# Performance work log

Hardware: AMD Instinct MI355X
Metric: run time of the kernel (lower is better)

The kernel has to match this reference:

```python
import jax, jax.numpy as jnp
import numpy as np
import math

HEAD_DIM = 128
NUM_HEADS = 16
ROPE_BASE = 10000.0


def _rope(x, st_pos):
    # x: [B, S, H, hd], interleaved even/odd rotation as in the torch module
    S, hd = x.shape[1], x.shape[3]
    theta = 1.0 / (ROPE_BASE ** (jnp.arange(0, hd, 2, dtype=jnp.float32) / hd))  # [hd/2]
    pos = jnp.arange(st_pos, st_pos + S, dtype=jnp.float32)[:, None]             # [S,1]
    ang = pos * theta                                                            # [S, hd/2]
    sin = jnp.sin(ang)[None, :, None, :]
    cos = jnp.cos(ang)[None, :, None, :]
    xe, xo = x[..., 0::2], x[..., 1::2]
    re = xe * cos - xo * sin
    ro = xe * sin + xo * cos
    # re-interleave: stack pairs then flatten last two dims
    return jnp.stack([re, ro], axis=-1).reshape(x.shape)


def setup_inputs() -> dict:
    key = jax.random.key(0)
    ks = jax.random.split(key, 6)
    B, S, D = 4, 2048, 2048
    scale = 1.0 / math.sqrt(D)
    x = jax.random.normal(ks[0], (B, S, D), dtype=jnp.float32)
    # causal additive mask (prefill)
    mask = jnp.where(jnp.tril(jnp.ones((S, S), dtype=bool)), 0.0, -1e9).astype(jnp.float32)
    Wq = jax.random.normal(ks[1], (D, NUM_HEADS * HEAD_DIM), dtype=jnp.float32) * scale
    Wk = jax.random.normal(ks[2], (D, NUM_HEADS * HEAD_DIM), dtype=jnp.float32) * scale
    Wv = jax.random.normal(ks[3], (D, NUM_HEADS * HEAD_DIM), dtype=jnp.float32) * scale
    Wo = jax.random.normal(ks[4], (NUM_HEADS * HEAD_DIM, D), dtype=jnp.float32) * scale
    return {"x": x, "mask": mask, "Wq": Wq, "Wk": Wk, "Wv": Wv, "Wo": Wo, "st_pos": 0}


def reference(x, mask, Wq, Wk, Wv, Wo, st_pos):
    B, S, D = x.shape
    H, hd = NUM_HEADS, HEAD_DIM
    q = (x @ Wq).reshape(B, S, H, hd)
    k = (x @ Wk).reshape(B, S, H, hd)
    v = (x @ Wv).reshape(B, S, H, hd)
    q = _rope(q, st_pos)
    k = _rope(k, st_pos)
    # st_pos=0 prefill: cache slice == current k, v; n_rep == 1 (n_kv_heads=num_heads)
    scores = jnp.einsum('bqhd,bkhd->bhqk', q, k) / math.sqrt(hd)
    if mask is not None:
        scores = scores + mask
    attn = jax.nn.softmax(scores, axis=-1)
    a = jnp.einsum('bhqk,bkhd->bqhd', attn, v).reshape(B, S, H * hd)
    return a @ Wo
```

## Files before the change

kernel.cpp:

```cpp
#include <hip/hip_runtime.h>
#include <hip/hip_fp16.h>

typedef _Float16 f16;
typedef __attribute__((ext_vector_type(2))) _Float16 f16x2;
typedef __attribute__((ext_vector_type(4))) _Float16 f16x4v;
typedef __attribute__((ext_vector_type(8))) _Float16 f16x8;
typedef __attribute__((ext_vector_type(4))) float f32x4;

#define DEV __device__ __forceinline__

static constexpr int S_ = 2048;
static constexpr int D_ = 2048;
static constexpr int H_ = 16;
static constexpr int HD_ = 128;
static constexpr int B_ = 4;

typedef const __attribute__((address_space(1))) void* gptr_t;
typedef __attribute__((address_space(3))) void* lptr_t;

DEV void gl_lds16(const void* gsrc, void* lds) {
  __builtin_amdgcn_global_load_lds((gptr_t)gsrc, (lptr_t)lds, 16, 0, 0);
}

__global__ __launch_bounds__(256) void cvt_f32_to_f16(const float* __restrict__ in,
                                                      f16* __restrict__ out, long n) {
  long i0 = ((long)blockIdx.x * 256 + threadIdx.x) * 4;
  long stride = (long)gridDim.x * 256 * 4;
  for (long i = i0; i < n; i += stride) {
    float4 v = *(const float4*)(in + i);
    f16x4v o;
    o[0] = (f16)v.x; o[1] = (f16)v.y; o[2] = (f16)v.z; o[3] = (f16)v.w;
    *(f16x4v*)(out + i) = o;
  }
}

__global__ __launch_bounds__(256) void wtrans4(const float* __restrict__ W0, const float* __restrict__ W1,
                                               const float* __restrict__ W2, const float* __restrict__ W3,
                                               f16* __restrict__ Wt) {
  __shared__ float tile[32][33];
  int wi = blockIdx.y;
  const float* W = wi == 0 ? W0 : wi == 1 ? W1 : wi == 2 ? W2 : W3;
  f16* dst = Wt + (size_t)wi * D_ * D_;
  int bx = blockIdx.x & 63, by = blockIdx.x >> 6;
  int r0 = by << 5, c0 = bx << 5;
  int tx = threadIdx.x & 31, ty = threadIdx.x >> 5;
#pragma unroll
  for (int i = 0; i < 4; i++) {
    int r = ty + i * 8;
    tile[r][tx] = W[(size_t)(r0 + r) * D_ + c0 + tx];
  }
  __syncthreads();
#pragma unroll
  for (int i = 0; i < 4; i++) {
    int r = ty + i * 8;
    dst[(size_t)(c0 + r) * D_ + r0 + tx] = (f16)tile[tx][r];
  }
}

DEV f16x8 lds_frag(const f16* half, int row, int s, int lg) {
  int byte = row * 128 + s * 64 + lg * 16;
  byte ^= (row & 4) << 3;
  return *(const f16x8*)((const char*)half + byte);
}

template <typename CT>
__global__ __launch_bounds__(512, 2) void gemm8(const f16* __restrict__ A, const f16* __restrict__ Bt,
                                                CT* __restrict__ C, int M, int N, int K) {
  __shared__ alignas(16) f16 As[2][2][128 * 64];
  __shared__ alignas(16) f16 Bs[2][2][128 * 64];
  int nbx = N >> 8;
  int nwg = (M >> 8) * nbx;
  int bid = blockIdx.x;
  int wg = (bid & 7) * (nwg >> 3) + (bid >> 3);
  int bx = wg % nbx, by = wg / nbx;
  int tid = threadIdx.x, w = tid >> 6, l = tid & 63;
  int wm = w >> 2, wn = w & 3, lg = l >> 4, ln = l & 15;
  int nt = K >> 6;
  const f16* Ab = A + (size_t)(by * 256) * K;
  const f16* Bb = Bt + (size_t)(bx * 256) * K;

  auto stage = [&](const f16* src0, int kt, f16* dst) {
#pragma unroll
    for (int j = 0; j < 2; j++) {
      int c = j * 8 + w;
      int row = c * 8 + (l >> 3);
      int scol = ((l & 7) * 8) ^ ((row & 4) << 2);
      gl_lds16(src0 + (size_t)row * K + kt * 64 + scol, (char*)dst + c * 1024);
    }
  };

  f32x4 acc[8][4] = {};

  stage(Ab, 0, As[0][0]);
  stage(Ab + (size_t)128 * K, 0, As[0][1]);
  stage(Bb, 0, Bs[0][0]);
  stage(Bb + (size_t)128 * K, 0, Bs[0][1]);
  if (nt > 1) {
    stage(Bb, 1, Bs[1][0]);
    stage(Bb + (size_t)128 * K, 1, Bs[1][1]);
  }

  for (int t = 0; t < nt; t++) {
    if (t + 2 < nt) asm volatile("s_waitcnt vmcnt(4)" ::: "memory");
    else            asm volatile("s_waitcnt vmcnt(0)" ::: "memory");
    __builtin_amdgcn_s_barrier();
    asm volatile("" ::: "memory");
    const f16* Ah = As[t & 1][wm];
    const f16* Bh = Bs[t & 1][wn >> 1];
    int br0 = (wn & 1) * 64;
    f16x8 a[4], b0[4], b1[4];
#pragma unroll
    for (int i = 0; i < 4; i++) a[i] = lds_frag(Ah, i * 16 + ln, 0, lg);
#pragma unroll
    for (int i = 0; i < 4; i++) b0[i] = lds_frag(Bh, br0 + i * 16 + ln, 0, lg);
    if (t + 1 < nt) stage(Ab, t + 1, As[(t + 1) & 1][0]);
    __builtin_amdgcn_s_barrier();
    asm volatile("" ::: "memory");
    __builtin_amdgcn_s_setprio(1);
#pragma unroll
    for (int mi = 0; mi < 4; mi++)
#pragma unroll
      for (int ni = 0; ni < 4; ni++)
        acc[mi][ni] = __builtin_amdgcn_mfma_f32_16x16x32_f16(a[mi], b0[ni], acc[mi][ni], 0, 0, 0);
    __builtin_amdgcn_s_setprio(0);
    __builtin_amdgcn_s_barrier();
    asm volatile("" ::: "memory");
#pragma unroll
    for (int i = 0; i < 4; i++) a[i] = lds_frag(Ah, i * 16 + ln, 1, lg);
#pragma unroll
    for (int i = 0; i < 4; i++) b1[i] = lds_frag(Bh, br0 + i * 16 + ln, 1, lg);
    if (t + 1 < nt) stage(Ab + (size_t)128 * K, t + 1, As[(t + 1) & 1][1]);
    __builtin_amdgcn_s_barrier();
    asm volatile("" ::: "memory");
    __builtin_amdgcn_s_setprio(1);
#pragma unroll
    for (int mi = 0; mi < 4; mi++)
#pragma unroll
      for (int ni = 0; ni < 4; ni++)
        acc[mi][ni] = __builtin_amdgcn_mfma_f32_16x16x32_f16(a[mi], b1[ni], acc[mi][ni], 0, 0, 0);
    __builtin_amdgcn_s_setprio(0);
    __builtin_amdgcn_s_barrier();
    asm volatile("" ::: "memory");
#pragma unroll
    for (int i = 0; i < 4; i++) a[i] = lds_frag(Ah, 64 + i * 16 + ln, 0, lg);
    if (t + 2 < nt) stage(Bb, t + 2, Bs[t & 1][0]);
    __builtin_amdgcn_s_barrier();
    asm volatile("" ::: "memory");
    __builtin_amdgcn_s_setprio(1);
#pragma unroll
    for (int mi = 0; mi < 4; mi++)
#pragma unroll
      for (int ni = 0; ni < 4; ni++)
        acc[mi + 4][ni] = __builtin_amdgcn_mfma_f32_16x16x32_f16(a[mi], b0[ni], acc[mi + 4][ni], 0, 0, 0);
    __builtin_amdgcn_s_setprio(0);
    __builtin_amdgcn_s_barrier();
    asm volatile("" ::: "memory");
#pragma unroll
    for (int i = 0; i < 4; i++) a[i] = lds_frag(Ah, 64 + i * 16 + ln, 1, lg);
    if (t + 2 < nt) stage(Bb + (size_t)128 * K, t + 2, Bs[t & 1][1]);
    __builtin_amdgcn_s_barrier();
    asm volatile("" ::: "memory");
    __builtin_amdgcn_s_setprio(1);
#pragma unroll
    for (int mi = 0; mi < 4; mi++)
#pragma unroll
      for (int ni = 0; ni < 4; ni++)
        acc[mi + 4][ni] = __builtin_amdgcn_mfma_f32_16x16x32_f16(a[mi], b1[ni], acc[mi + 4][ni], 0, 0, 0);
    __builtin_amdgcn_s_setprio(0);
    __builtin_amdgcn_s_barrier();
    asm volatile("" ::: "memory");
  }

  int row0 = by * 256 + wm * 128;
  int col0 = bx * 256 + wn * 64;
#pragma unroll
  for (int mi = 0; mi < 8; mi++)
#pragma unroll
    for (int ni = 0; ni < 4; ni++)
#pragma unroll
      for (int r4 = 0; r4 < 4; r4++) {
        int row = row0 + mi * 16 + lg * 4 + r4;
        int col = col0 + ni * 16 + ln;
        float o = acc[mi][ni][r4];
        if constexpr (sizeof(CT) == 2) {
          float oo = __shfl_xor(o, 1);
          if (!(ln & 1)) {
            f16x2 pp; pp[0] = (f16)o; pp[1] = (f16)oo;
            *(f16x2*)(&C[(size_t)row * N + col]) = pp;
          }
        } else {
          C[(size_t)row * N + col] = o;
        }
      }
}

__global__ __launch_bounds__(256) void rope_table(float2* __restrict__ tab, const int* __restrict__ st) {
  int i = blockIdx.x * 256 + threadIdx.x;
  int s = i >> 6, j = i & 63;
  float theta = powf(10000.f, -(float)j / 64.f);
  float ang = (float)(s + st[0]) * theta;
  tab[i] = make_float2(cosf(ang), sinf(ang));
}

__global__ __launch_bounds__(256) void rope_apply(f16* __restrict__ X, const float2* __restrict__ tab,
                                                  float scale, long npairs) {
  long i0 = (long)blockIdx.x * 256 + threadIdx.x;
  long stride = (long)gridDim.x * 256;
  for (long p = i0; p < npairs; p += stride) {
    long row = p >> 10;
    int jp = (int)(p & 1023);
    int s = (int)(row & (S_ - 1));
    float2 cs = tab[s * 64 + (jp & 63)];
    f16x2 v = *(const f16x2*)(X + 2 * p);
    float xe = (float)v[0], xo = (float)v[1];
    float re = (xe * cs.x - xo * cs.y) * scale;
    float ro = (xe * cs.y + xo * cs.x) * scale;
    f16x2 o; o[0] = (f16)re; o[1] = (f16)ro;
    *(f16x2*)(X + 2 * p) = o;
  }
}

__global__ __launch_bounds__(256) void vtrans2(const f16* __restrict__ V, f16* __restrict__ VT2) {
  __shared__ alignas(16) f16 tile[64 * 128];
  int t = blockIdx.x, bh = blockIdx.y, b = bh >> 4, h = bh & 15;
  int tid = threadIdx.x, w = tid >> 6, l = tid & 63, lg = l >> 4, ln = l & 15;
  const f16* src = V + ((size_t)(b * S_ + t * 64) * H_ + h) * HD_;
#pragma unroll
  for (int i = 0; i < 4; i++) {
    int idx = i * 256 + tid;
    int r = idx >> 4, c8 = idx & 15;
    int c8s = c8 ^ ((r >> 3) & 3);
    *(f16x8*)(&tile[r * 128 + c8s * 8]) = *(const f16x8*)(src + (size_t)r * (H_ * HD_) + c8 * 8);
  }
  __syncthreads();
  f16* dst = VT2 + (size_t)(bh * 32 + t) * 16 * 512;
#pragma unroll
  for (int ci = 0; ci < 4; ci++) {
    int c = w * 4 + ci;
    int nj = c >> 1, kk = c & 1;
    f16x8 v;
#pragma unroll
    for (int e = 0; e < 8; e++) {
      int r = kk * 32 + lg * 8 + e;
      int col = nj * 16 + ln;
      int c8s = (col >> 3) ^ ((r >> 3) & 3);
      v[e] = tile[r * 128 + c8s * 8 + (col & 7)];
    }
    *(f16x8*)(dst + (size_t)c * 512 + l * 8) = v;
  }
}

__global__ __launch_bounds__(512, 4) void attn(const f16* __restrict__ Q, const f16* __restrict__ K,
                                               const f16* __restrict__ VT2, f16* __restrict__ O,
                                               const float2* __restrict__ tab) {
  __shared__ alignas(16) f16 kls[2][64 * 128];
  int id = blockIdx.x;
  int r8 = id & 7, j = id >> 3;
  int u = j & 7, g = j >> 3;
  int bh = r8 + (g << 3);
  int b = bh >> 4, h = bh & 15;
  int tid = threadIdx.x, w = tid >> 6, l = tid & 63, lg = l >> 4, ln = l & 15;

  const float QSCALE = 0.12751744910173355f;
  const f16* kp = K + (size_t)(b * S_) * D_ + h * HD_;
  const f16* vp2 = VT2 + (size_t)bh * 32 * 16 * 512;

  auto stageK = [&](int buf, int kv0) {
#pragma unroll
    for (int jj = 0; jj < 2; jj++) {
      int i = jj * 8 + w;
      int byte = i * 1024 + 16 * l;
      int r = byte >> 8;
      int c = ((byte >> 4) & 15) ^ (r & 7);
      gl_lds16(kp + (size_t)(kv0 + r) * D_ + c * 8, (char*)kls[buf] + i * 1024);
    }
  };

  int slo = ln + (((lg * 2) & 3) << 4);
  int shi = ln + (((lg * 2 + 1) & 3) << 4);
  int sel = (lg >> 1) & 1;

#pragma unroll 1
  for (int pi = 0; pi < 2; pi++) {
    int qsel = pi ? u : 15 - u;
    int q0 = qsel << 7;
    int qrow = q0 + w * 16 + ln;
    const f16* qp = Q + (size_t)(b * S_ + qrow) * D_ + h * HD_;
    const float2* tq = tab + (size_t)qrow * 64;
    f16x8 qf[4];
#pragma unroll
    for (int kc = 0; kc < 4; kc++) {
      f16x8 q = *(const f16x8*)(qp + kc * 32 + lg * 8);
#pragma unroll
      for (int p = 0; p < 4; p++) {
        float2 cs = tq[kc * 16 + lg * 4 + p];
        float e0 = (float)q[2 * p], e1 = (float)q[2 * p + 1];
        q[2 * p] = (f16)((e0 * cs.x - e1 * cs.y) * QSCALE);
        q[2 * p + 1] = (f16)((e0 * cs.y + e1 * cs.x) * QSCALE);
      }
      qf[kc] = q;
    }

    float m = -1e30f, lsum = 0.f;
    f32x4 oacc[8] = {};

    int nt = (q0 >> 6) + 2;
    if (pi) __syncthreads();
    stageK(0, 0);
    for (int t = 0; t < nt; t++) {
      int kv0 = t << 6;
      int cur = t & 1;
      __syncthreads();
      if (t + 1 < nt) stageK(cur ^ 1, (t + 1) << 6);
      if (kv0 > q0 + w * 16 + 15) continue;
      const f16* kb = kls[cur];
      const f16* vt = vp2 + (size_t)t * 16 * 512;

      f16x8 vfa[8];
#pragma unroll
      for (int c = 0; c < 8; c++) vfa[c] = *(const f16x8*)(vt + c * 512 + l * 8);

      f32x4 sf[4];
      __builtin_amdgcn_s_setprio(1);
#pragma unroll
      for (int ni = 0; ni < 4; ni++) {
        int n = ni * 16 + ln;
        f32x4 s = {0.f, 0.f, 0.f, 0.f};
#pragma unroll
        for (int kc = 0; kc < 4; kc++) {
          int mch = kc * 4 + lg;
          f16x8 kf = *(const f16x8*)(&kb[n * 128 + ((mch ^ (n & 7)) << 3)]);
          s = __builtin_amdgcn_mfma_f32_16x16x32_f16(kf, qf[kc], s, 0, 0, 0);
        }
        sf[ni] = s;
      }
      __builtin_amdgcn_s_setprio(0);

      if (t >= nt - 2) {
#pragma unroll
        for (int ni = 0; ni < 4; ni++) {
          int kvg = kv0 + ni * 16 + lg * 4;
#pragma unroll
          for (int r4 = 0; r4 < 4; r4++)
            if (kvg + r4 > qrow) sf[ni][r4] = -1e30f;
        }
      }
      float pm = fmaxf(fmaxf(fmaxf(sf[0][0], sf[0][1]), fmaxf(sf[0][2], sf[0][3])),
                       fmaxf(fmaxf(sf[1][0], sf[1][1]), fmaxf(sf[1][2], sf[1][3])));
      pm = fmaxf(pm, fmaxf(fmaxf(fmaxf(sf[2][0], sf[2][1]), fmaxf(sf[2][2], sf[2][3])),
                           fmaxf(fmaxf(sf[3][0], sf[3][1]), fmaxf(sf[3][2], sf[3][3]))));
      pm = fmaxf(pm, __shfl_xor(pm, 16));
      pm = fmaxf(pm, __shfl_xor(pm, 32));
      float scl = 1.f;
      bool defer = __all(pm <= m + 8.f);
      if (!defer) {
        float mn = fmaxf(m, pm);
        scl = __builtin_amdgcn_exp2f(m - mn);
        m = mn;
      }
      float rsum = 0.f;
#pragma unroll
      for (int ni = 0; ni < 4; ni++)
#pragma unroll
        for (int r4 = 0; r4 < 4; r4++) {
          float p = __builtin_amdgcn_exp2f(sf[ni][r4] - m);
          sf[ni][r4] = p;
          rsum += p;
        }
      lsum = lsum * scl + rsum;

      f16x4v hp[4];
#pragma unroll
      for (int ni = 0; ni < 4; ni++) {
        hp[ni][0] = (f16)sf[ni][0]; hp[ni][1] = (f16)sf[ni][1];
        hp[ni][2] = (f16)sf[ni][2]; hp[ni][3] = (f16)sf[ni][3];
      }
      if (!defer) {
#pragma unroll
        for (int nj = 0; nj < 8; nj++)
#pragma unroll
          for (int r4 = 0; r4 < 4; r4++) oacc[nj][r4] *= scl;
      }

      f16x8 pa[2];
#pragma unroll
      for (int kk = 0; kk < 2; kk++) {
        int2 e = __builtin_bit_cast(int2, hp[2 * kk]);
        int2 o = __builtin_bit_cast(int2, hp[2 * kk + 1]);
        int t0x = __shfl(e.x, slo), t0y = __shfl(e.y, slo);
        int t1x = __shfl(o.x, slo), t1y = __shfl(o.y, slo);
        int t2x = __shfl(e.x, shi), t2y = __shfl(e.y, shi);
        int t3x = __shfl(o.x, shi), t3y = __shfl(o.y, shi);
        int2 lo, hi;
        lo.x = sel ? t1x : t0x; lo.y = sel ? t1y : t0y;
        hi.x = sel ? t3x : t2x; hi.y = sel ? t3y : t2y;
        f16x4v plo = __builtin_bit_cast(f16x4v, lo);
        f16x4v phi = __builtin_bit_cast(f16x4v, hi);
        f16x8 p;
        p[0] = plo[0]; p[1] = plo[1]; p[2] = plo[2]; p[3] = plo[3];
        p[4] = phi[0]; p[5] = phi[1]; p[6] = phi[2]; p[7] = phi[3];
        pa[kk] = p;
      }

      __builtin_amdgcn_s_setprio(1);
#pragma unroll
      for (int kk = 0; kk < 2; kk++)
#pragma unroll
        for (int nj = 0; nj < 4; nj++)
          oacc[nj] = __builtin_amdgcn_mfma_f32_16x16x32_f16(vfa[nj * 2 + kk], pa[kk], oacc[nj], 0, 0, 0);
#pragma unroll
      for (int njb = 0; njb < 2; njb++) {
        f16x8 vf[4];
#pragma unroll
        for (int jj = 0; jj < 2; jj++)
#pragma unroll
          for (int kk = 0; kk < 2; kk++)
            vf[jj * 2 + kk] = *(const f16x8*)(vt + (size_t)(((4 + njb * 2 + jj) * 2 + kk) * 512) + l * 8);
#pragma unroll
        for (int kk = 0; kk < 2; kk++)
#pragma unroll
          for (int jj = 0; jj < 2; jj++)
            oacc[4 + njb * 2 + jj] = __builtin_amdgcn_mfma_f32_16x16x32_f16(
                vf[jj * 2 + kk], pa[kk], oacc[4 + njb * 2 + jj], 0, 0, 0);
      }
      __builtin_amdgcn_s_setprio(0);
    }

    lsum += __shfl_xor(lsum, 16);
    lsum += __shfl_xor(lsum, 32);
    f16* op = O + (size_t)(b * S_ + qrow) * D_ + h * HD_;
    float inv = 1.f / lsum;
#pragma unroll
    for (int nj = 0; nj < 8; nj++) {
      f16x4v ov;
#pragma unroll
      for (int r4 = 0; r4 < 4; r4++) ov[r4] = (f16)(oacc[nj][r4] * inv);
      *(f16x4v*)(op + nj * 16 + lg * 4) = ov;
    }
  }
}

extern "C" void kernel_launch(void* const* d_in, const int* in_sizes, int n_in,
                              void* d_out, int out_size, void* d_ws, size_t ws_size,
                              hipStream_t stream) {
  (void)in_sizes; (void)n_in; (void)out_size; (void)ws_size;
  const float* x = (const float*)d_in[0];
  const float* Wq = (const float*)d_in[2];
  const float* Wk = (const float*)d_in[3];
  const float* Wv = (const float*)d_in[4];
  const float* Wo = (const float*)d_in[5];
  const int* stp = (const int*)d_in[6];
  float* out = (float*)d_out;

  const size_t MS = (size_t)B_ * S_;
  f16* xh = (f16*)d_ws;
  f16* wqt = xh + MS * D_;
  f16* wkt = wqt + (size_t)D_ * D_;
  f16* wvt = wkt + (size_t)D_ * D_;
  f16* wot = wvt + (size_t)D_ * D_;
  f16* qh = wot + (size_t)D_ * D_;
  f16* kh = qh + MS * D_;
  f16* vh = kh + MS * D_;
  float2* tab = (float2*)(vh + MS * D_);
  f16* vt2 = xh;
  f16* aoh = vh;

  cvt_f32_to_f16<<<16384, 256, 0, stream>>>(x, xh, (long)(MS * D_));
  wtrans4<<<dim3(4096, 4), 256, 0, stream>>>(Wq, Wk, Wv, Wo, wqt);
  gemm8<f16><<<256, 512, 0, stream>>>(xh, wqt, qh, 8192, 2048, 2048);
  gemm8<f16><<<256, 512, 0, stream>>>(xh, wkt, kh, 8192, 2048, 2048);
  gemm8<f16><<<256, 512, 0, stream>>>(xh, wvt, vh, 8192, 2048, 2048);
  rope_table<<<512, 256, 0, stream>>>(tab, stp);
  rope_apply<<<4096, 256, 0, stream>>>(kh, tab, 1.0f, (long)(MS * 1024));
  vtrans2<<<dim3(32, 64), 256, 0, stream>>>(vh, vt2);
  attn<<<512, 512, 0, stream>>>(qh, kh, vt2, aoh, tab);
  gemm8<float><<<256, 512, 0, stream>>>(aoh, wot, out, 8192, 2048, 2048);
}
```

Measured before the change: 474.3 us.

## Fuse K RoPE into GEMM epilogue and load K directly from global in attention

```diff
diff --git a/kernel.cpp b/kernel.cpp
--- a/kernel.cpp
+++ b/kernel.cpp
@@ -20,6 +20,10 @@
 
 DEV void gl_lds16(const void* gsrc, void* lds) {
   __builtin_amdgcn_global_load_lds((gptr_t)gsrc, (lptr_t)lds, 16, 0, 0);
+}
+
+DEV int cvt_pk_i32(float a, float b) {
+  return __builtin_bit_cast(int, __builtin_amdgcn_cvt_pkrtz(a, b));
 }
 
 __global__ __launch_bounds__(256) void cvt_f32_to_f16(const float* __restrict__ in,
@@ -63,9 +67,10 @@
   return *(const f16x8*)((const char*)half + byte);
 }
 
-template <typename CT>
+template <typename CT, bool ROPE>
 __global__ __launch_bounds__(512, 2) void gemm8(const f16* __restrict__ A, const f16* __restrict__ Bt,
-                                                CT* __restrict__ C, int M, int N, int K) {
+                                                CT* __restrict__ C, int M, int N, int K,
+                                                const float2* __restrict__ tab) {
   __shared__ alignas(16) f16 As[2][2][128 * 64];
   __shared__ alignas(16) f16 Bs[2][2][128 * 64];
   int nbx = N >> 8;
@@ -185,7 +190,16 @@
         if constexpr (sizeof(CT) == 2) {
           float oo = __shfl_xor(o, 1);
           if (!(ln & 1)) {
-            f16x2 pp; pp[0] = (f16)o; pp[1] = (f16)oo;
+            f16x2 pp;
+            if constexpr (ROPE) {
+              int s = row & (S_ - 1);
+              int jp = (col & 127) >> 1;
+              float2 cs = tab[s * 64 + jp];
+              pp[0] = (f16)(o * cs.x - oo * cs.y);
+              pp[1] = (f16)(o * cs.y + oo * cs.x);
+            } else {
+              pp[0] = (f16)o; pp[1] = (f16)oo;
+            }
             *(f16x2*)(&C[(size_t)row * N + col]) = pp;
           }
         } else {
@@ -200,24 +214,6 @@
   float theta = powf(10000.f, -(float)j / 64.f);
   float ang = (float)(s + st[0]) * theta;
   tab[i] = make_float2(cosf(ang), sinf(ang));
-}
-
-__global__ __launch_bounds__(256) void rope_apply(f16* __restrict__ X, const float2* __restrict__ tab,
-                                                  float scale, long npairs) {
-  long i0 = (long)blockIdx.x * 256 + threadIdx.x;
-  long stride = (long)gridDim.x * 256;
-  for (long p = i0; p < npairs; p += stride) {
-    long row = p >> 10;
-    int jp = (int)(p & 1023);
-    int s = (int)(row & (S_ - 1));
-    float2 cs = tab[s * 64 + (jp & 63)];
-    f16x2 v = *(const f16x2*)(X + 2 * p);
-    float xe = (float)v[0], xo = (float)v[1];
-    float re = (xe * cs.x - xo * cs.y) * scale;
-    float ro = (xe * cs.y + xo * cs.x) * scale;
-    f16x2 o; o[0] = (f16)re; o[1] = (f16)ro;
-    *(f16x2*)(X + 2 * p) = o;
-  }
 }
 
 __global__ __launch_bounds__(256) void vtrans2(const f16* __restrict__ V, f16* __restrict__ VT2) {
@@ -253,7 +249,6 @@
 __global__ __launch_bounds__(512, 4) void attn(const f16* __restrict__ Q, const f16* __restrict__ K,
                                                const f16* __restrict__ VT2, f16* __restrict__ O,
                                                const float2* __restrict__ tab) {
-  __shared__ alignas(16) f16 kls[2][64 * 128];
   int id = blockIdx.x;
   int r8 = id & 7, j = id >> 3;
   int u = j & 7, g = j >> 3;
@@ -264,17 +259,6 @@
   const float QSCALE = 0.12751744910173355f;
   const f16* kp = K + (size_t)(b * S_) * D_ + h * HD_;
   const f16* vp2 = VT2 + (size_t)bh * 32 * 16 * 512;
-
-  auto stageK = [&](int buf, int kv0) {
-#pragma unroll
-    for (int jj = 0; jj < 2; jj++) {
-      int i = jj * 8 + w;
-      int byte = i * 1024 + 16 * l;
-      int r = byte >> 8;
-      int c = ((byte >> 4) & 15) ^ (r & 7);
-      gl_lds16(kp + (size_t)(kv0 + r) * D_ + c * 8, (char*)kls[buf] + i * 1024);
-    }
-  };
 
   int slo = ln + (((lg * 2) & 3) << 4);
   int shi = ln + (((lg * 2 + 1) & 3) << 4);
@@ -304,39 +288,35 @@
     float m = -1e30f, lsum = 0.f;
     f32x4 oacc[8] = {};
 
-    int nt = (q0 >> 6) + 2;
-    if (pi) __syncthreads();
-    stageK(0, 0);
-    for (int t = 0; t < nt; t++) {
+    int wnt = ((q0 + w * 16 + 15) >> 6) + 1;
+    for (int t = 0; t < wnt; t++) {
       int kv0 = t << 6;
-      int cur = t & 1;
-      __syncthreads();
-      if (t + 1 < nt) stageK(cur ^ 1, (t + 1) << 6);
-      if (kv0 > q0 + w * 16 + 15) continue;
-      const f16* kb = kls[cur];
       const f16* vt = vp2 + (size_t)t * 16 * 512;
 
       f16x8 vfa[8];
 #pragma unroll
-      for (int c = 0; c < 8; c++) vfa[c] = *(const f16x8*)(vt + c * 512 + l * 8);
+      for (int c = 0; c < 4; c++) vfa[c] = *(const f16x8*)(vt + c * 512 + l * 8);
 
       f32x4 sf[4];
+#pragma unroll
+      for (int ni = 0; ni < 4; ni++) sf[ni] = f32x4{0.f, 0.f, 0.f, 0.f};
       __builtin_amdgcn_s_setprio(1);
 #pragma unroll
-      for (int ni = 0; ni < 4; ni++) {
-        int n = ni * 16 + ln;
-        f32x4 s = {0.f, 0.f, 0.f, 0.f};
-#pragma unroll
-        for (int kc = 0; kc < 4; kc++) {
-          int mch = kc * 4 + lg;
-          f16x8 kf = *(const f16x8*)(&kb[n * 128 + ((mch ^ (n & 7)) << 3)]);
-          s = __builtin_amdgcn_mfma_f32_16x16x32_f16(kf, qf[kc], s, 0, 0, 0);
-        }
-        sf[ni] = s;
+      for (int kc = 0; kc < 4; kc++) {
+        f16x8 kf[4];
+#pragma unroll
+        for (int ni = 0; ni < 4; ni++)
+          kf[ni] = *(const f16x8*)(kp + (size_t)(kv0 + ni * 16 + ln) * D_ + (kc * 4 + lg) * 8);
+#pragma unroll
+        for (int ni = 0; ni < 4; ni++)
+          sf[ni] = __builtin_amdgcn_mfma_f32_16x16x32_f16(kf[ni], qf[kc], sf[ni], 0, 0, 0);
       }
       __builtin_amdgcn_s_setprio(0);
 
-      if (t >= nt - 2) {
+#pragma unroll
+      for (int c = 4; c < 8; c++) vfa[c] = *(const f16x8*)(vt + c * 512 + l * 8);
+
+      if (t == wnt - 1) {
 #pragma unroll
         for (int ni = 0; ni < 4; ni++) {
           int kvg = kv0 + ni * 16 + lg * 4;
@@ -369,12 +349,6 @@
         }
       lsum = lsum * scl + rsum;
 
-      f16x4v hp[4];
-#pragma unroll
-      for (int ni = 0; ni < 4; ni++) {
-        hp[ni][0] = (f16)sf[ni][0]; hp[ni][1] = (f16)sf[ni][1];
-        hp[ni][2] = (f16)sf[ni][2]; hp[ni][3] = (f16)sf[ni][3];
-      }
       if (!defer) {
 #pragma unroll
         for (int nj = 0; nj < 8; nj++)
@@ -385,12 +359,14 @@
       f16x8 pa[2];
 #pragma unroll
       for (int kk = 0; kk < 2; kk++) {
-        int2 e = __builtin_bit_cast(int2, hp[2 * kk]);
-        int2 o = __builtin_bit_cast(int2, hp[2 * kk + 1]);
-        int t0x = __shfl(e.x, slo), t0y = __shfl(e.y, slo);
-        int t1x = __shfl(o.x, slo), t1y = __shfl(o.y, slo);
-        int t2x = __shfl(e.x, shi), t2y = __shfl(e.y, shi);
-        int t3x = __shfl(o.x, shi), t3y = __shfl(o.y, shi);
+        int ex = cvt_pk_i32(sf[2 * kk][0], sf[2 * kk][1]);
+        int ey = cvt_pk_i32(sf[2 * kk][2], sf[2 * kk][3]);
+        int ox = cvt_pk_i32(sf[2 * kk + 1][0], sf[2 * kk + 1][1]);
+        int oy = cvt_pk_i32(sf[2 * kk + 1][2], sf[2 * kk + 1][3]);
+        int t0x = __shfl(ex, slo), t0y = __shfl(ey, slo);
+        int t1x = __shfl(ox, slo), t1y = __shfl(oy, slo);
+        int t2x = __shfl(ex, shi), t2y = __shfl(ey, shi);
+        int t3x = __shfl(ox, shi), t3y = __shfl(oy, shi);
         int2 lo, hi;
         lo.x = sel ? t1x : t0x; lo.y = sel ? t1y : t0y;
         hi.x = sel ? t3x : t2x; hi.y = sel ? t3y : t2y;
@@ -467,12 +443,11 @@
 
   cvt_f32_to_f16<<<16384, 256, 0, stream>>>(x, xh, (long)(MS * D_));
   wtrans4<<<dim3(4096, 4), 256, 0, stream>>>(Wq, Wk, Wv, Wo, wqt);
-  gemm8<f16><<<256, 512, 0, stream>>>(xh, wqt, qh, 8192, 2048, 2048);
-  gemm8<f16><<<256, 512, 0, stream>>>(xh, wkt, kh, 8192, 2048, 2048);
-  gemm8<f16><<<256, 512, 0, stream>>>(xh, wvt, vh, 8192, 2048, 2048);
   rope_table<<<512, 256, 0, stream>>>(tab, stp);
-  rope_apply<<<4096, 256, 0, stream>>>(kh, tab, 1.0f, (long)(MS * 1024));
+  gemm8<f16, false><<<256, 512, 0, stream>>>(xh, wqt, qh, 8192, 2048, 2048, nullptr);
+  gemm8<f16, true><<<256, 512, 0, stream>>>(xh, wkt, kh, 8192, 2048, 2048, tab);
+  gemm8<f16, false><<<256, 512, 0, stream>>>(xh, wvt, vh, 8192, 2048, 2048, nullptr);
   vtrans2<<<dim3(32, 64), 256, 0, stream>>>(vh, vt2);
   attn<<<512, 512, 0, stream>>>(qh, kh, vt2, aoh, tab);
-  gemm8<float><<<256, 512, 0, stream>>>(aoh, wot, out, 8192, 2048, 2048);
-}
+  gemm8<float, false><<<256, 512, 0, stream>>>(aoh, wot, out, 8192, 2048, 2048, nullptr);
+}
```

Result: slower. 663.5 us (+39.9%).

## Permute V transpose layout to drop P shuffles, rotate K LDS swizzle

Applied to the files above, without the earlier changes.

```diff
diff --git a/kernel.cpp b/kernel.cpp
--- a/kernel.cpp
+++ b/kernel.cpp
@@ -6,6 +6,7 @@
 typedef __attribute__((ext_vector_type(4))) _Float16 f16x4v;
 typedef __attribute__((ext_vector_type(8))) _Float16 f16x8;
 typedef __attribute__((ext_vector_type(4))) float f32x4;
+typedef __attribute__((ext_vector_type(4))) int i32x4;
 
 #define DEV __device__ __forceinline__
 
@@ -20,6 +21,10 @@
 
 DEV void gl_lds16(const void* gsrc, void* lds) {
   __builtin_amdgcn_global_load_lds((gptr_t)gsrc, (lptr_t)lds, 16, 0, 0);
+}
+
+DEV int cvt_pk_i32(float a, float b) {
+  return __builtin_bit_cast(int, __builtin_amdgcn_cvt_pkrtz(a, b));
 }
 
 __global__ __launch_bounds__(256) void cvt_f32_to_f16(const float* __restrict__ in,
@@ -241,7 +246,7 @@
     f16x8 v;
 #pragma unroll
     for (int e = 0; e < 8; e++) {
-      int r = kk * 32 + lg * 8 + e;
+      int r = 16 * (2 * kk + (e >> 2)) + 4 * lg + (e & 3);
       int col = nj * 16 + ln;
       int c8s = (col >> 3) ^ ((r >> 3) & 3);
       v[e] = tile[r * 128 + c8s * 8 + (col & 7)];
@@ -271,14 +276,10 @@
       int i = jj * 8 + w;
       int byte = i * 1024 + 16 * l;
       int r = byte >> 8;
-      int c = ((byte >> 4) & 15) ^ (r & 7);
+      int c = (((byte >> 4) & 15) - r) & 15;
       gl_lds16(kp + (size_t)(kv0 + r) * D_ + c * 8, (char*)kls[buf] + i * 1024);
     }
   };
-
-  int slo = ln + (((lg * 2) & 3) << 4);
-  int shi = ln + (((lg * 2 + 1) & 3) << 4);
-  int sel = (lg >> 1) & 1;
 
 #pragma unroll 1
   for (int pi = 0; pi < 2; pi++) {
@@ -316,10 +317,6 @@
       const f16* kb = kls[cur];
       const f16* vt = vp2 + (size_t)t * 16 * 512;
 
-      f16x8 vfa[8];
-#pragma unroll
-      for (int c = 0; c < 8; c++) vfa[c] = *(const f16x8*)(vt + c * 512 + l * 8);
-
       f32x4 sf[4];
       __builtin_amdgcn_s_setprio(1);
 #pragma unroll
@@ -329,12 +326,16 @@
 #pragma unroll
         for (int kc = 0; kc < 4; kc++) {
           int mch = kc * 4 + lg;
-          f16x8 kf = *(const f16x8*)(&kb[n * 128 + ((mch ^ (n & 7)) << 3)]);
+          f16x8 kf = *(const f16x8*)(&kb[n * 128 + (((mch + n) & 15) << 3)]);
           s = __builtin_amdgcn_mfma_f32_16x16x32_f16(kf, qf[kc], s, 0, 0, 0);
         }
         sf[ni] = s;
       }
       __builtin_amdgcn_s_setprio(0);
+
+      f16x8 vfa[8];
+#pragma unroll
+      for (int c = 0; c < 8; c++) vfa[c] = *(const f16x8*)(vt + c * 512 + l * 8);
 
       if (t >= nt - 2) {
 #pragma unroll
@@ -369,12 +370,6 @@
         }
       lsum = lsum * scl + rsum;
 
-      f16x4v hp[4];
-#pragma unroll
-      for (int ni = 0; ni < 4; ni++) {
-        hp[ni][0] = (f16)sf[ni][0]; hp[ni][1] = (f16)sf[ni][1];
-        hp[ni][2] = (f16)sf[ni][2]; hp[ni][3] = (f16)sf[ni][3];
-      }
       if (!defer) {
 #pragma unroll
         for (int nj = 0; nj < 8; nj++)
@@ -385,21 +380,12 @@
       f16x8 pa[2];
 #pragma unroll
       for (int kk = 0; kk < 2; kk++) {
-        int2 e = __builtin_bit_cast(int2, hp[2 * kk]);
-        int2 o = __builtin_bit_cast(int2, hp[2 * kk + 1]);
-        int t0x = __shfl(e.x, slo), t0y = __shfl(e.y, slo);
-        int t1x = __shfl(o.x, slo), t1y = __shfl(o.y, slo);
-        int t2x = __shfl(e.x, shi), t2y = __shfl(e.y, shi);
-        int t3x = __shfl(o.x, shi), t3y = __shfl(o.y, shi);
-        int2 lo, hi;
-        lo.x = sel ? t1x : t0x; lo.y = sel ? t1y : t0y;
-        hi.x = sel ? t3x : t2x; hi.y = sel ? t3y : t2y;
-        f16x4v plo = __builtin_bit_cast(f16x4v, lo);
-        f16x4v phi = __builtin_bit_cast(f16x4v, hi);
-        f16x8 p;
-        p[0] = plo[0]; p[1] = plo[1]; p[2] = plo[2]; p[3] = plo[3];
-        p[4] = phi[0]; p[5] = phi[1]; p[6] = phi[2]; p[7] = phi[3];
-        pa[kk] = p;
+        i32x4 wv;
+        wv.x = cvt_pk_i32(sf[2 * kk][0], sf[2 * kk][1]);
+        wv.y = cvt_pk_i32(sf[2 * kk][2], sf[2 * kk][3]);
+        wv.z = cvt_pk_i32(sf[2 * kk + 1][0], sf[2 * kk + 1][1]);
+        wv.w = cvt_pk_i32(sf[2 * kk + 1][2], sf[2 * kk + 1][3]);
+        pa[kk] = __builtin_bit_cast(f16x8, wv);
       }
 
       __builtin_amdgcn_s_setprio(1);
```

Result: no change. 467.2 us (-1.5%).
